# Optimization experiments

Hardware: AMD Instinct MI355X
Metric: run time of the kernel (lower is better)

The kernel has to match this reference:

```python
import jax, jax.numpy as jnp
import numpy as np

AGENT_RADIUS = 0.3
B, F, H1, H21, H22, C, K = 262144, 5, 128, 32, 32, 2, 8


def _linear_init(k, fan_in, fan_out):
    lim = 1.0 / np.sqrt(fan_in)
    kw, kb = jax.random.split(k)
    W = jax.random.uniform(kw, (fan_out, fan_in), jnp.float32, -lim, lim)
    b = jax.random.uniform(kb, (fan_out,), jnp.float32, -lim, lim)
    return W, b


def setup_inputs() -> dict:
    key = jax.random.key(0)
    ks = jax.random.split(key, 9)
    W1, b1 = _linear_init(ks[0], F, H1)
    W21, b21 = _linear_init(ks[1], H1, H21)
    W22, b22 = _linear_init(ks[2], H1, H22)
    W31, b31 = _linear_init(ks[3], H21, C)
    W32, b32 = _linear_init(ks[4], H22, C)
    x = jax.random.normal(ks[5], (B, F), jnp.float32)
    mean = jax.random.normal(ks[6], (F,), jnp.float32) * 0.1
    std = jax.random.uniform(ks[7], (F,), jnp.float32, 0.5, 1.5)
    obs_xy = jax.random.uniform(ks[8], (K, 2), jnp.float32, -10.0, 10.0)
    obstacles = jnp.concatenate([obs_xy, jnp.full((K, 1), 0.5, jnp.float32)], axis=1)  # [K,3] = (ox,oy,r)
    return {"x": x, "mean": mean, "std": std,
            "W1": W1, "b1": b1, "W21": W21, "b21": b21, "W22": W22, "b22": b22,
            "W31": W31, "b31": b31, "W32": W32, "b32": b32,
            "obstacles": obstacles, "sgn": 1}


def _barriernet(x, mean, std, W1, b1, W21, b21, W22, b22, W31, b31, W32, b32, obstacles):
    nB = x.shape[0]
    x0 = x * std + mean
    h1 = jax.nn.relu(x @ W1.T + b1)                 # [B, H1]
    x21 = jax.nn.relu(h1 @ W21.T + b21)             # [B, H21]
    x22 = jax.nn.relu(h1 @ W22.T + b22)             # [B, H22]
    x31 = x21 @ W31.T + b31                          # [B, 2]  QP linear term p
    x32 = 4.0 * jax.nn.sigmoid(x22 @ W32.T + b32)    # [B, 2]  CBF class-K gains

    xo = x0 * std + mean  # module denormalizes twice inside dCBF (faithful to source)
    px, py, theta = xo[:, 0], xo[:, 1], xo[:, 2]
    oppx, oppy = xo[:, 3], xo[:, 4]
    cos_t, sin_t = jnp.cos(theta), jnp.sin(theta)

    # K static obstacles (broadcast) + 1 per-sample opponent -> nobs = K+1
    ox = jnp.concatenate([jnp.broadcast_to(obstacles[:, 0], (nB, K)), oppx[:, None]], axis=1)
    oy = jnp.concatenate([jnp.broadcast_to(obstacles[:, 1], (nB, K)), oppy[:, None]], axis=1)
    orr = jnp.concatenate([jnp.broadcast_to(obstacles[:, 2], (nB, K)),
                           jnp.full((nB, 1), AGENT_RADIUS, x.dtype)], axis=1)
    dx = px[:, None] - ox                            # [B, nobs]
    dy = py[:, None] - oy
    barrier = dx * dx + dy * dy - orr * orr          # [B, nobs]
    LgLf1 = 2.0 * dx * cos_t[:, None] + 2.0 * dy * sin_t[:, None]

    # QP: min 0.5 u^T I u + p^T u  s.t.  g1*u1 <= h  (second G column is 0)
    g1 = -LgLf1                                      # [B, nobs]
    hvec = (x32[:, 0] * x32[:, 1])[:, None] * barrier
    safe_g = jnp.where(g1 != 0.0, g1, 1.0)
    ratio = hvec / safe_g
    upper = jnp.min(jnp.where(g1 > 0.0, ratio, jnp.inf), axis=1)   # tightest u1 upper bound
    lower = jnp.max(jnp.where(g1 < 0.0, ratio, -jnp.inf), axis=1)  # tightest u1 lower bound
    u1 = jnp.clip(-x31[:, 0], lower, upper)          # exact KKT solution of the 1-D QP
    u2 = -x31[:, 1]                                  # unconstrained coordinate
    return jnp.stack([u1, u2], axis=1)               # [B, 2]


def reference(x, mean, std, W1, b1, W21, b21, W22, b22, W31, b31, W32, b32, obstacles, sgn):
    return _barriernet(x, mean, std, W1, b1, W21, b21, W22, b22, W31, b31, W32, b32, obstacles)
```

## Files before the change

### kernel.cpp

```cpp
#include <hip/hip_runtime.h>
#include <math.h>

typedef __attribute__((ext_vector_type(8))) short short8v;
typedef __attribute__((ext_vector_type(4))) float f32x4;

#define BLOCK 256
#define GRID  512

__device__ inline unsigned int pk_bf16(float lo, float hi) {
    unsigned int r;
    asm("v_cvt_pk_bf16_f32 %0, %1, %2" : "=v"(r) : "v"(lo), "v"(hi));
    return r;
}
__device__ inline short8v as_s8(uint4 v) { union { uint4 u; short8v s; } c; c.u = v; return c.s; }
__device__ inline f32x4 as_f4(float4 v) { union { float4 u; f32x4 s; } c; c.u = v; return c.s; }

__global__ __launch_bounds__(BLOCK, 2) void bnet(
    const float* __restrict__ x,
    const float* __restrict__ meanp, const float* __restrict__ stdp,
    const float* __restrict__ W1,  const float* __restrict__ b1,
    const float* __restrict__ W21, const float* __restrict__ b21,
    const float* __restrict__ W22, const float* __restrict__ b22,
    const float* __restrict__ W31, const float* __restrict__ b31,
    const float* __restrict__ W32, const float* __restrict__ b32,
    const float* __restrict__ obstacles,
    float* __restrict__ out, int nB)
{
    __shared__ uint4 w1frag[8 * 64];
    __shared__ uint4 fragB[16 * 64];
    __shared__ uint4 headA[2 * 64];
    __shared__ float b2s[64];

    const int t = threadIdx.x;

    {
        uint4 z = {0u, 0u, 0u, 0u};
        w1frag[t] = z; w1frag[t + 256] = z;
    }
    __syncthreads();
    if (t < 128) {
        int m = t & 15, g = t >> 4;
        int u = 16 * g + m;
        const float* wr = W1 + u * 5;
        uint4 v;
        v.x = pk_bf16(wr[0], wr[1]);
        v.y = pk_bf16(wr[2], wr[3]);
        v.z = pk_bf16(wr[4], b1[u]);
        v.w = 0u;
        w1frag[g * 64 + m] = v;
    } else {
        int e  = t - 128;
        int ks = e >> 6, l = e & 63, m = l & 15, qq = l >> 4;
        float v[8];
        #pragma unroll
        for (int j = 0; j < 8; ++j) {
            int u = 16 * ((j >> 2) & 1) + 4 * qq + (j & 3);
            float val = 0.f;
            if (m == 0 && ks == 0) val = W31[u];
            if (m == 1 && ks == 0) val = W31[32 + u];
            if (m == 2 && ks == 1) val = W32[u];
            if (m == 3 && ks == 1) val = W32[32 + u];
            v[j] = val;
        }
        uint4 h;
        h.x = pk_bf16(v[0], v[1]); h.y = pk_bf16(v[2], v[3]);
        h.z = pk_bf16(v[4], v[5]); h.w = pk_bf16(v[6], v[7]);
        headA[ks * 64 + l] = h;
    }
    if (t < 64) b2s[t] = (t < 32) ? b21[t] : b22[t - 32];
    {
        const float4* w21v = (const float4*)W21;
        const float4* w22v = (const float4*)W22;
        #pragma unroll
        for (int e = 0; e < 4; ++e) {
            int g4   = t + e * 256;
            int uo   = g4 >> 5;
            int h0   = (g4 & 31) << 2;
            int ks   = h0 >> 5;
            int jh   = (h0 >> 4) & 1;
            int qq   = (h0 >> 2) & 3;
            int ln   = (qq << 4) | (uo & 15);
            int half = uo >> 4;
            float4 f1 = w21v[g4];
            float4 f2 = w22v[g4];
            unsigned int* dA = (unsigned int*)&fragB[(half * 4 + ks) * 64 + ln];
            unsigned int* dB = (unsigned int*)&fragB[(8 + half * 4 + ks) * 64 + ln];
            dA[jh * 2] = pk_bf16(f1.x, f1.y); dA[jh * 2 + 1] = pk_bf16(f1.z, f1.w);
            dB[jh * 2] = pk_bf16(f2.x, f2.y); dB[jh * 2 + 1] = pk_bf16(f2.z, f2.w);
        }
    }
    __syncthreads();

    const int lane = t & 63;
    const int q    = lane >> 4;
    const int r15  = lane & 15;
    const int wid    = blockIdx.x * 4 + (t >> 6);
    const int nwaves = GRID * 4;
    const int npairs = (nB + 31) >> 5;
    if (wid >= npairs) return;

    short8v bfr[16];
    #pragma unroll
    for (int i = 0; i < 16; ++i) bfr[i] = as_s8(fragB[i * 64 + lane]);
    const short8v hA0 = as_s8(headA[lane]);
    const short8v hA1 = as_s8(headA[64 + lane]);
    const float4* b2v = (const float4*)b2s;

    const float hb0 = b31[0], hb1 = b31[1], hb2 = b32[0], hb3 = b32[1];

    auto MLP = [&](const float xA[5], const float xB[5], f32x4& hdA, f32x4& hdB) {
        uint4 va, vb;
        va.x = pk_bf16(xA[0], xA[1]); va.y = pk_bf16(xA[2], xA[3]);
        va.z = pk_bf16(xA[4], 1.0f);  va.w = 0u;
        vb.x = pk_bf16(xB[0], xB[1]); vb.y = pk_bf16(xB[2], xB[3]);
        vb.z = pk_bf16(xB[4], 1.0f);  vb.w = 0u;
        short8v xfA = as_s8(va), xfB = as_s8(vb);

        short8v afA[4], afB[4];
        #pragma unroll
        for (int ks = 0; ks < 4; ++ks) {
            f32x4 z = {0.f, 0.f, 0.f, 0.f};
            short8v w0  = as_s8(w1frag[(2 * ks) * 64 + lane]);
            short8v w1v = as_s8(w1frag[(2 * ks + 1) * 64 + lane]);
            f32x4 hA0_ = __builtin_amdgcn_mfma_f32_16x16x32_bf16(w0,  xfA, z, 0, 0, 0);
            f32x4 hA1_ = __builtin_amdgcn_mfma_f32_16x16x32_bf16(w1v, xfA, z, 0, 0, 0);
            f32x4 hB0_ = __builtin_amdgcn_mfma_f32_16x16x32_bf16(w0,  xfB, z, 0, 0, 0);
            f32x4 hB1_ = __builtin_amdgcn_mfma_f32_16x16x32_bf16(w1v, xfB, z, 0, 0, 0);
            uint4 pa, pb;
            pa.x = pk_bf16(fmaxf(hA0_[0], 0.f), fmaxf(hA0_[1], 0.f));
            pa.y = pk_bf16(fmaxf(hA0_[2], 0.f), fmaxf(hA0_[3], 0.f));
            pa.z = pk_bf16(fmaxf(hA1_[0], 0.f), fmaxf(hA1_[1], 0.f));
            pa.w = pk_bf16(fmaxf(hA1_[2], 0.f), fmaxf(hA1_[3], 0.f));
            pb.x = pk_bf16(fmaxf(hB0_[0], 0.f), fmaxf(hB0_[1], 0.f));
            pb.y = pk_bf16(fmaxf(hB0_[2], 0.f), fmaxf(hB0_[3], 0.f));
            pb.z = pk_bf16(fmaxf(hB1_[0], 0.f), fmaxf(hB1_[1], 0.f));
            pb.w = pk_bf16(fmaxf(hB1_[2], 0.f), fmaxf(hB1_[3], 0.f));
            afA[ks] = as_s8(pa); afB[ks] = as_s8(pb);
        }

        f32x4 a21aA = as_f4(b2v[q]);
        f32x4 a21bA = as_f4(b2v[4 + q]);
        f32x4 a22aA = as_f4(b2v[8 + q]);
        f32x4 a22bA = as_f4(b2v[12 + q]);
        f32x4 a21aB = a21aA, a21bB = a21bA, a22aB = a22aA, a22bB = a22bA;
        #pragma unroll
        for (int ks = 0; ks < 4; ++ks) {
            a21aA = __builtin_amdgcn_mfma_f32_16x16x32_bf16(bfr[     ks], afA[ks], a21aA, 0, 0, 0);
            a21aB = __builtin_amdgcn_mfma_f32_16x16x32_bf16(bfr[     ks], afB[ks], a21aB, 0, 0, 0);
            a21bA = __builtin_amdgcn_mfma_f32_16x16x32_bf16(bfr[ 4 + ks], afA[ks], a21bA, 0, 0, 0);
            a21bB = __builtin_amdgcn_mfma_f32_16x16x32_bf16(bfr[ 4 + ks], afB[ks], a21bB, 0, 0, 0);
            a22aA = __builtin_amdgcn_mfma_f32_16x16x32_bf16(bfr[ 8 + ks], afA[ks], a22aA, 0, 0, 0);
            a22aB = __builtin_amdgcn_mfma_f32_16x16x32_bf16(bfr[ 8 + ks], afB[ks], a22aB, 0, 0, 0);
            a22bA = __builtin_amdgcn_mfma_f32_16x16x32_bf16(bfr[12 + ks], afA[ks], a22bA, 0, 0, 0);
            a22bB = __builtin_amdgcn_mfma_f32_16x16x32_bf16(bfr[12 + ks], afB[ks], a22bB, 0, 0, 0);
        }

        uint4 h1A, h2A, h1B, h2B;
        h1A.x = pk_bf16(fmaxf(a21aA[0], 0.f), fmaxf(a21aA[1], 0.f));
        h1A.y = pk_bf16(fmaxf(a21aA[2], 0.f), fmaxf(a21aA[3], 0.f));
        h1A.z = pk_bf16(fmaxf(a21bA[0], 0.f), fmaxf(a21bA[1], 0.f));
        h1A.w = pk_bf16(fmaxf(a21bA[2], 0.f), fmaxf(a21bA[3], 0.f));
        h2A.x = pk_bf16(fmaxf(a22aA[0], 0.f), fmaxf(a22aA[1], 0.f));
        h2A.y = pk_bf16(fmaxf(a22aA[2], 0.f), fmaxf(a22aA[3], 0.f));
        h2A.z = pk_bf16(fmaxf(a22bA[0], 0.f), fmaxf(a22bA[1], 0.f));
        h2A.w = pk_bf16(fmaxf(a22bA[2], 0.f), fmaxf(a22bA[3], 0.f));
        h1B.x = pk_bf16(fmaxf(a21aB[0], 0.f), fmaxf(a21aB[1], 0.f));
        h1B.y = pk_bf16(fmaxf(a21aB[2], 0.f), fmaxf(a21aB[3], 0.f));
        h1B.z = pk_bf16(fmaxf(a21bB[0], 0.f), fmaxf(a21bB[1], 0.f));
        h1B.w = pk_bf16(fmaxf(a21bB[2], 0.f), fmaxf(a21bB[3], 0.f));
        h2B.x = pk_bf16(fmaxf(a22aB[0], 0.f), fmaxf(a22aB[1], 0.f));
        h2B.y = pk_bf16(fmaxf(a22aB[2], 0.f), fmaxf(a22aB[3], 0.f));
        h2B.z = pk_bf16(fmaxf(a22bB[0], 0.f), fmaxf(a22bB[1], 0.f));
        h2B.w = pk_bf16(fmaxf(a22bB[2], 0.f), fmaxf(a22bB[3], 0.f));

        f32x4 ini = {hb0, hb1, hb2, hb3};
        hdA = __builtin_amdgcn_mfma_f32_16x16x32_bf16(hA0, as_s8(h1A), ini, 0, 0, 0);
        hdA = __builtin_amdgcn_mfma_f32_16x16x32_bf16(hA1, as_s8(h2A), hdA, 0, 0, 0);
        hdB = __builtin_amdgcn_mfma_f32_16x16x32_bf16(hA0, as_s8(h1B), ini, 0, 0, 0);
        hdB = __builtin_amdgcn_mfma_f32_16x16x32_bf16(hA1, as_s8(h2B), hdB, 0, 0, 0);
    };

    auto LOADX = [&](int p, float xA[5], float xB[5]) {
        int rA = p * 32 + r15;      if (rA >= nB) rA = nB - 1;
        int rB = p * 32 + 16 + r15; if (rB >= nB) rB = nB - 1;
        const float* pA = x + (size_t)rA * 5;
        const float* pB = x + (size_t)rB * 5;
        #pragma unroll
        for (int c = 0; c < 5; ++c) { xA[c] = pA[c]; xB[c] = pB[c]; }
    };

    int p = wid;
    float xrA[5], xrB[5];
    LOADX(p, xrA, xrB);
    f32x4 hdA, hdB;
    MLP(xrA, xrB, hdA, hdB);

    while (true) {
        const int nxt = p + nwaves;
        const bool has = nxt < npairs;
        float xnA[5], xnB[5];
        if (has) LOADX(nxt, xnA, xnB);

        {
            float hs0 = __shfl(hdB[0], r15);
            float hs1 = __shfl(hdB[1], r15);
            float hs2 = __shfl(hdB[2], r15);
            float hs3 = __shfl(hdB[3], r15);
            if (lane < 32) {
                const bool sa = (lane < 16);
                float x31_0 = sa ? hdA[0] : hs0;
                float x31_1 = sa ? hdA[1] : hs1;
                float t32_0 = sa ? hdA[2] : hs2;
                float t32_1 = sa ? hdA[3] : hs3;

                float s0v = __fdividef(4.f, 1.f + __expf(-t32_0));
                float s1v = __fdividef(4.f, 1.f + __expf(-t32_1));
                float hcoef = s0v * s1v;

                float xo[5];
                #pragma unroll
                for (int c = 0; c < 5; ++c) {
                    float m = meanp[c], s = stdp[c];
                    float xc = sa ? xrA[c] : xrB[c];
                    float x0 = fmaf(xc, s, m);
                    xo[c] = fmaf(x0, s, m);
                }
                float px = xo[0], py = xo[1], th = xo[2], oppx = xo[3], oppy = xo[4];
                float st, ct;
                __sincosf(th, &st, &ct);

                float upper = INFINITY, lower = -INFINITY;
                #pragma unroll
                for (int j = 0; j < 9; ++j) {
                    float ox, oy, rr2;
                    if (j < 8) {
                        ox = obstacles[j * 3];
                        oy = obstacles[j * 3 + 1];
                        float rr = obstacles[j * 3 + 2];
                        rr2 = rr * rr;
                    } else {
                        ox = oppx; oy = oppy; rr2 = 0.3f * 0.3f;
                    }
                    float dx = px - ox, dy = py - oy;
                    float bar = fmaf(dx, dx, fmaf(dy, dy, -rr2));
                    float g1  = -2.f * fmaf(dx, ct, dy * st);
                    float ratio = __fdividef(hcoef * bar, (g1 != 0.f) ? g1 : 1.f);
                    if (g1 > 0.f) upper = fminf(upper, ratio);
                    if (g1 < 0.f) lower = fmaxf(lower, ratio);
                }
                float u1 = fminf(fmaxf(-x31_0, lower), upper);
                float u2 = -x31_1;

                int row = p * 32 + lane;
                if (row < nB) {
                    float2 o; o.x = u1; o.y = u2;
                    *reinterpret_cast<float2*>(out + 2 * (size_t)row) = o;
                }
            }
        }

        if (!has) break;
        MLP(xnA, xnB, hdA, hdB);
        p = nxt;
        #pragma unroll
        for (int c = 0; c < 5; ++c) { xrA[c] = xnA[c]; xrB[c] = xnB[c]; }
    }
}

extern "C" void kernel_launch(void* const* d_in, const int* in_sizes, int n_in,
                              void* d_out, int out_size, void* d_ws, size_t ws_size,
                              hipStream_t stream) {
    const float* x         = (const float*)d_in[0];
    const float* meanp     = (const float*)d_in[1];
    const float* stdp      = (const float*)d_in[2];
    const float* W1        = (const float*)d_in[3];
    const float* b1        = (const float*)d_in[4];
    const float* W21       = (const float*)d_in[5];
    const float* b21       = (const float*)d_in[6];
    const float* W22       = (const float*)d_in[7];
    const float* b22       = (const float*)d_in[8];
    const float* W31       = (const float*)d_in[9];
    const float* b31       = (const float*)d_in[10];
    const float* W32       = (const float*)d_in[11];
    const float* b32       = (const float*)d_in[12];
    const float* obstacles = (const float*)d_in[13];
    float* out = (float*)d_out;

    int nB = in_sizes[0] / 5;
    bnet<<<GRID, BLOCK, 0, stream>>>(
        x, meanp, stdp, W1, b1, W21, b21, W22, b22,
        W31, b31, W32, b32, obstacles, out, nB);
}
```

Baseline: 19.79 us.

## Unroll persistent loop into four fixed pairs with two-pair batched MLP

Replaces the persistent while-loop with a straight-line schedule in which each wave handles exactly four 32-row pairs. The MLP now runs two pairs at once, interleaving the first and second layers per k-step, and epilogues are interleaved with the next MLP batch. The aim is more independent MFMA chains in flight (more ILP) and less loop and prefetch overhead. It raises accumulator register pressure, and it silently assumes the batch needs at most four pairs per wave, so larger inputs would leave rows uncomputed.

```diff
diff --git a/kernel.cpp b/kernel.cpp
--- a/kernel.cpp
+++ b/kernel.cpp
@@ -102,83 +102,11 @@
     short8v bfr[16];
     #pragma unroll
     for (int i = 0; i < 16; ++i) bfr[i] = as_s8(fragB[i * 64 + lane]);
-    const short8v hA0 = as_s8(headA[lane]);
-    const short8v hA1 = as_s8(headA[64 + lane]);
+    const short8v hfr0 = as_s8(headA[lane]);
+    const short8v hfr1 = as_s8(headA[64 + lane]);
     const float4* b2v = (const float4*)b2s;
 
     const float hb0 = b31[0], hb1 = b31[1], hb2 = b32[0], hb3 = b32[1];
-
-    auto MLP = [&](const float xA[5], const float xB[5], f32x4& hdA, f32x4& hdB) {
-        uint4 va, vb;
-        va.x = pk_bf16(xA[0], xA[1]); va.y = pk_bf16(xA[2], xA[3]);
-        va.z = pk_bf16(xA[4], 1.0f);  va.w = 0u;
-        vb.x = pk_bf16(xB[0], xB[1]); vb.y = pk_bf16(xB[2], xB[3]);
-        vb.z = pk_bf16(xB[4], 1.0f);  vb.w = 0u;
-        short8v xfA = as_s8(va), xfB = as_s8(vb);
-
-        short8v afA[4], afB[4];
-        #pragma unroll
-        for (int ks = 0; ks < 4; ++ks) {
-            f32x4 z = {0.f, 0.f, 0.f, 0.f};
-            short8v w0  = as_s8(w1frag[(2 * ks) * 64 + lane]);
-            short8v w1v = as_s8(w1frag[(2 * ks + 1) * 64 + lane]);
-            f32x4 hA0_ = __builtin_amdgcn_mfma_f32_16x16x32_bf16(w0,  xfA, z, 0, 0, 0);
-            f32x4 hA1_ = __builtin_amdgcn_mfma_f32_16x16x32_bf16(w1v, xfA, z, 0, 0, 0);
-            f32x4 hB0_ = __builtin_amdgcn_mfma_f32_16x16x32_bf16(w0,  xfB, z, 0, 0, 0);
-            f32x4 hB1_ = __builtin_amdgcn_mfma_f32_16x16x32_bf16(w1v, xfB, z, 0, 0, 0);
-            uint4 pa, pb;
-            pa.x = pk_bf16(fmaxf(hA0_[0], 0.f), fmaxf(hA0_[1], 0.f));
-            pa.y = pk_bf16(fmaxf(hA0_[2], 0.f), fmaxf(hA0_[3], 0.f));
-            pa.z = pk_bf16(fmaxf(hA1_[0], 0.f), fmaxf(hA1_[1], 0.f));
-            pa.w = pk_bf16(fmaxf(hA1_[2], 0.f), fmaxf(hA1_[3], 0.f));
-            pb.x = pk_bf16(fmaxf(hB0_[0], 0.f), fmaxf(hB0_[1], 0.f));
-            pb.y = pk_bf16(fmaxf(hB0_[2], 0.f), fmaxf(hB0_[3], 0.f));
-            pb.z = pk_bf16(fmaxf(hB1_[0], 0.f), fmaxf(hB1_[1], 0.f));
-            pb.w = pk_bf16(fmaxf(hB1_[2], 0.f), fmaxf(hB1_[3], 0.f));
-            afA[ks] = as_s8(pa); afB[ks] = as_s8(pb);
-        }
-
-        f32x4 a21aA = as_f4(b2v[q]);
-        f32x4 a21bA = as_f4(b2v[4 + q]);
-        f32x4 a22aA = as_f4(b2v[8 + q]);
-        f32x4 a22bA = as_f4(b2v[12 + q]);
-        f32x4 a21aB = a21aA, a21bB = a21bA, a22aB = a22aA, a22bB = a22bA;
-        #pragma unroll
-        for (int ks = 0; ks < 4; ++ks) {
-            a21aA = __builtin_amdgcn_mfma_f32_16x16x32_bf16(bfr[     ks], afA[ks], a21aA, 0, 0, 0);
-            a21aB = __builtin_amdgcn_mfma_f32_16x16x32_bf16(bfr[     ks], afB[ks], a21aB, 0, 0, 0);
-            a21bA = __builtin_amdgcn_mfma_f32_16x16x32_bf16(bfr[ 4 + ks], afA[ks], a21bA, 0, 0, 0);
-            a21bB = __builtin_amdgcn_mfma_f32_16x16x32_bf16(bfr[ 4 + ks], afB[ks], a21bB, 0, 0, 0);
-            a22aA = __builtin_amdgcn_mfma_f32_16x16x32_bf16(bfr[ 8 + ks], afA[ks], a22aA, 0, 0, 0);
-            a22aB = __builtin_amdgcn_mfma_f32_16x16x32_bf16(bfr[ 8 + ks], afB[ks], a22aB, 0, 0, 0);
-            a22bA = __builtin_amdgcn_mfma_f32_16x16x32_bf16(bfr[12 + ks], afA[ks], a22bA, 0, 0, 0);
-            a22bB = __builtin_amdgcn_mfma_f32_16x16x32_bf16(bfr[12 + ks], afB[ks], a22bB, 0, 0, 0);
-        }
-
-        uint4 h1A, h2A, h1B, h2B;
-        h1A.x = pk_bf16(fmaxf(a21aA[0], 0.f), fmaxf(a21aA[1], 0.f));
-        h1A.y = pk_bf16(fmaxf(a21aA[2], 0.f), fmaxf(a21aA[3], 0.f));
-        h1A.z = pk_bf16(fmaxf(a21bA[0], 0.f), fmaxf(a21bA[1], 0.f));
-        h1A.w = pk_bf16(fmaxf(a21bA[2], 0.f), fmaxf(a21bA[3], 0.f));
-        h2A.x = pk_bf16(fmaxf(a22aA[0], 0.f), fmaxf(a22aA[1], 0.f));
-        h2A.y = pk_bf16(fmaxf(a22aA[2], 0.f), fmaxf(a22aA[3], 0.f));
-        h2A.z = pk_bf16(fmaxf(a22bA[0], 0.f), fmaxf(a22bA[1], 0.f));
-        h2A.w = pk_bf16(fmaxf(a22bA[2], 0.f), fmaxf(a22bA[3], 0.f));
-        h1B.x = pk_bf16(fmaxf(a21aB[0], 0.f), fmaxf(a21aB[1], 0.f));
-        h1B.y = pk_bf16(fmaxf(a21aB[2], 0.f), fmaxf(a21aB[3], 0.f));
-        h1B.z = pk_bf16(fmaxf(a21bB[0], 0.f), fmaxf(a21bB[1], 0.f));
-        h1B.w = pk_bf16(fmaxf(a21bB[2], 0.f), fmaxf(a21bB[3], 0.f));
-        h2B.x = pk_bf16(fmaxf(a22aB[0], 0.f), fmaxf(a22aB[1], 0.f));
-        h2B.y = pk_bf16(fmaxf(a22aB[2], 0.f), fmaxf(a22aB[3], 0.f));
-        h2B.z = pk_bf16(fmaxf(a22bB[0], 0.f), fmaxf(a22bB[1], 0.f));
-        h2B.w = pk_bf16(fmaxf(a22bB[2], 0.f), fmaxf(a22bB[3], 0.f));
-
-        f32x4 ini = {hb0, hb1, hb2, hb3};
-        hdA = __builtin_amdgcn_mfma_f32_16x16x32_bf16(hA0, as_s8(h1A), ini, 0, 0, 0);
-        hdA = __builtin_amdgcn_mfma_f32_16x16x32_bf16(hA1, as_s8(h2A), hdA, 0, 0, 0);
-        hdB = __builtin_amdgcn_mfma_f32_16x16x32_bf16(hA0, as_s8(h1B), ini, 0, 0, 0);
-        hdB = __builtin_amdgcn_mfma_f32_16x16x32_bf16(hA1, as_s8(h2B), hdB, 0, 0, 0);
-    };
 
     auto LOADX = [&](int p, float xA[5], float xB[5]) {
         int rA = p * 32 + r15;      if (rA >= nB) rA = nB - 1;
@@ -189,82 +117,209 @@
         for (int c = 0; c < 5; ++c) { xA[c] = pA[c]; xB[c] = pB[c]; }
     };
 
-    int p = wid;
-    float xrA[5], xrB[5];
-    LOADX(p, xrA, xrB);
-    f32x4 hdA, hdB;
-    MLP(xrA, xrB, hdA, hdB);
-
-    while (true) {
-        const int nxt = p + nwaves;
-        const bool has = nxt < npairs;
-        float xnA[5], xnB[5];
-        if (has) LOADX(nxt, xnA, xnB);
-
+    auto MLP4 = [&](const float xA0[5], const float xB0[5],
+                    const float xA1[5], const float xB1[5],
+                    f32x4& hd0A, f32x4& hd0B, f32x4& hd1A, f32x4& hd1B) {
+        uint4 t0a, t0b, t1a, t1b;
+        t0a.x = pk_bf16(xA0[0], xA0[1]); t0a.y = pk_bf16(xA0[2], xA0[3]);
+        t0a.z = pk_bf16(xA0[4], 1.0f);   t0a.w = 0u;
+        t0b.x = pk_bf16(xB0[0], xB0[1]); t0b.y = pk_bf16(xB0[2], xB0[3]);
+        t0b.z = pk_bf16(xB0[4], 1.0f);   t0b.w = 0u;
+        t1a.x = pk_bf16(xA1[0], xA1[1]); t1a.y = pk_bf16(xA1[2], xA1[3]);
+        t1a.z = pk_bf16(xA1[4], 1.0f);   t1a.w = 0u;
+        t1b.x = pk_bf16(xB1[0], xB1[1]); t1b.y = pk_bf16(xB1[2], xB1[3]);
+        t1b.z = pk_bf16(xB1[4], 1.0f);   t1b.w = 0u;
+        short8v xf0A = as_s8(t0a), xf0B = as_s8(t0b);
+        short8v xf1A = as_s8(t1a), xf1B = as_s8(t1b);
+
+        f32x4 i0 = as_f4(b2v[q]),     i1 = as_f4(b2v[4 + q]);
+        f32x4 i2 = as_f4(b2v[8 + q]), i3 = as_f4(b2v[12 + q]);
+        f32x4 A0_21a = i0, A0_21b = i1, A0_22a = i2, A0_22b = i3;
+        f32x4 B0_21a = i0, B0_21b = i1, B0_22a = i2, B0_22b = i3;
+        f32x4 A1_21a = i0, A1_21b = i1, A1_22a = i2, A1_22b = i3;
+        f32x4 B1_21a = i0, B1_21b = i1, B1_22a = i2, B1_22b = i3;
+
+        #pragma unroll
+        for (int ks = 0; ks < 4; ++ks) {
+            f32x4 z = {0.f, 0.f, 0.f, 0.f};
+            short8v w0  = as_s8(w1frag[(2 * ks) * 64 + lane]);
+            short8v w1v = as_s8(w1frag[(2 * ks + 1) * 64 + lane]);
+            f32x4 u0A = __builtin_amdgcn_mfma_f32_16x16x32_bf16(w0,  xf0A, z, 0, 0, 0);
+            f32x4 v0A = __builtin_amdgcn_mfma_f32_16x16x32_bf16(w1v, xf0A, z, 0, 0, 0);
+            f32x4 u0B = __builtin_amdgcn_mfma_f32_16x16x32_bf16(w0,  xf0B, z, 0, 0, 0);
+            f32x4 v0B = __builtin_amdgcn_mfma_f32_16x16x32_bf16(w1v, xf0B, z, 0, 0, 0);
+            f32x4 u1A = __builtin_amdgcn_mfma_f32_16x16x32_bf16(w0,  xf1A, z, 0, 0, 0);
+            f32x4 v1A = __builtin_amdgcn_mfma_f32_16x16x32_bf16(w1v, xf1A, z, 0, 0, 0);
+            f32x4 u1B = __builtin_amdgcn_mfma_f32_16x16x32_bf16(w0,  xf1B, z, 0, 0, 0);
+            f32x4 v1B = __builtin_amdgcn_mfma_f32_16x16x32_bf16(w1v, xf1B, z, 0, 0, 0);
+            uint4 pa, pb, pc, pd;
+            pa.x = pk_bf16(fmaxf(u0A[0], 0.f), fmaxf(u0A[1], 0.f));
+            pa.y = pk_bf16(fmaxf(u0A[2], 0.f), fmaxf(u0A[3], 0.f));
+            pa.z = pk_bf16(fmaxf(v0A[0], 0.f), fmaxf(v0A[1], 0.f));
+            pa.w = pk_bf16(fmaxf(v0A[2], 0.f), fmaxf(v0A[3], 0.f));
+            pb.x = pk_bf16(fmaxf(u0B[0], 0.f), fmaxf(u0B[1], 0.f));
+            pb.y = pk_bf16(fmaxf(u0B[2], 0.f), fmaxf(u0B[3], 0.f));
+            pb.z = pk_bf16(fmaxf(v0B[0], 0.f), fmaxf(v0B[1], 0.f));
+            pb.w = pk_bf16(fmaxf(v0B[2], 0.f), fmaxf(v0B[3], 0.f));
+            pc.x = pk_bf16(fmaxf(u1A[0], 0.f), fmaxf(u1A[1], 0.f));
+            pc.y = pk_bf16(fmaxf(u1A[2], 0.f), fmaxf(u1A[3], 0.f));
+            pc.z = pk_bf16(fmaxf(v1A[0], 0.f), fmaxf(v1A[1], 0.f));
+            pc.w = pk_bf16(fmaxf(v1A[2], 0.f), fmaxf(v1A[3], 0.f));
+            pd.x = pk_bf16(fmaxf(u1B[0], 0.f), fmaxf(u1B[1], 0.f));
+            pd.y = pk_bf16(fmaxf(u1B[2], 0.f), fmaxf(u1B[3], 0.f));
+            pd.z = pk_bf16(fmaxf(v1B[0], 0.f), fmaxf(v1B[1], 0.f));
+            pd.w = pk_bf16(fmaxf(v1B[2], 0.f), fmaxf(v1B[3], 0.f));
+            short8v af0A = as_s8(pa), af0B = as_s8(pb);
+            short8v af1A = as_s8(pc), af1B = as_s8(pd);
+            A0_21a = __builtin_amdgcn_mfma_f32_16x16x32_bf16(bfr[     ks], af0A, A0_21a, 0, 0, 0);
+            B0_21a = __builtin_amdgcn_mfma_f32_16x16x32_bf16(bfr[     ks], af0B, B0_21a, 0, 0, 0);
+            A1_21a = __builtin_amdgcn_mfma_f32_16x16x32_bf16(bfr[     ks], af1A, A1_21a, 0, 0, 0);
+            B1_21a = __builtin_amdgcn_mfma_f32_16x16x32_bf16(bfr[     ks], af1B, B1_21a, 0, 0, 0);
+            A0_21b = __builtin_amdgcn_mfma_f32_16x16x32_bf16(bfr[ 4 + ks], af0A, A0_21b, 0, 0, 0);
+            B0_21b = __builtin_amdgcn_mfma_f32_16x16x32_bf16(bfr[ 4 + ks], af0B, B0_21b, 0, 0, 0);
+            A1_21b = __builtin_amdgcn_mfma_f32_16x16x32_bf16(bfr[ 4 + ks], af1A, A1_21b, 0, 0, 0);
+            B1_21b = __builtin_amdgcn_mfma_f32_16x16x32_bf16(bfr[ 4 + ks], af1B, B1_21b, 0, 0, 0);
+            A0_22a = __builtin_amdgcn_mfma_f32_16x16x32_bf16(bfr[ 8 + ks], af0A, A0_22a, 0, 0, 0);
+            B0_22a = __builtin_amdgcn_mfma_f32_16x16x32_bf16(bfr[ 8 + ks], af0B, B0_22a, 0, 0, 0);
+            A1_22a = __builtin_amdgcn_mfma_f32_16x16x32_bf16(bfr[ 8 + ks], af1A, A1_22a, 0, 0, 0);
+            B1_22a = __builtin_amdgcn_mfma_f32_16x16x32_bf16(bfr[ 8 + ks], af1B, B1_22a, 0, 0, 0);
+            A0_22b = __builtin_amdgcn_mfma_f32_16x16x32_bf16(bfr[12 + ks], af0A, A0_22b, 0, 0, 0);
+            B0_22b = __builtin_amdgcn_mfma_f32_16x16x32_bf16(bfr[12 + ks], af0B, B0_22b, 0, 0, 0);
+            A1_22b = __builtin_amdgcn_mfma_f32_16x16x32_bf16(bfr[12 + ks], af1A, A1_22b, 0, 0, 0);
+            B1_22b = __builtin_amdgcn_mfma_f32_16x16x32_bf16(bfr[12 + ks], af1B, B1_22b, 0, 0, 0);
+        }
+
+        f32x4 ini = {hb0, hb1, hb2, hb3};
         {
-            float hs0 = __shfl(hdB[0], r15);
-            float hs1 = __shfl(hdB[1], r15);
-            float hs2 = __shfl(hdB[2], r15);
-            float hs3 = __shfl(hdB[3], r15);
-            if (lane < 32) {
-                const bool sa = (lane < 16);
-                float x31_0 = sa ? hdA[0] : hs0;
-                float x31_1 = sa ? hdA[1] : hs1;
-                float t32_0 = sa ? hdA[2] : hs2;
-                float t32_1 = sa ? hdA[3] : hs3;
-
-                float s0v = __fdividef(4.f, 1.f + __expf(-t32_0));
-                float s1v = __fdividef(4.f, 1.f + __expf(-t32_1));
-                float hcoef = s0v * s1v;
-
-                float xo[5];
-                #pragma unroll
-                for (int c = 0; c < 5; ++c) {
-                    float m = meanp[c], s = stdp[c];
-                    float xc = sa ? xrA[c] : xrB[c];
-                    float x0 = fmaf(xc, s, m);
-                    xo[c] = fmaf(x0, s, m);
+            uint4 h1, h2;
+            h1.x = pk_bf16(fmaxf(A0_21a[0], 0.f), fmaxf(A0_21a[1], 0.f));
+            h1.y = pk_bf16(fmaxf(A0_21a[2], 0.f), fmaxf(A0_21a[3], 0.f));
+            h1.z = pk_bf16(fmaxf(A0_21b[0], 0.f), fmaxf(A0_21b[1], 0.f));
+            h1.w = pk_bf16(fmaxf(A0_21b[2], 0.f), fmaxf(A0_21b[3], 0.f));
+            h2.x = pk_bf16(fmaxf(A0_22a[0], 0.f), fmaxf(A0_22a[1], 0.f));
+            h2.y = pk_bf16(fmaxf(A0_22a[2], 0.f), fmaxf(A0_22a[3], 0.f));
+            h2.z = pk_bf16(fmaxf(A0_22b[0], 0.f), fmaxf(A0_22b[1], 0.f));
+            h2.w = pk_bf16(fmaxf(A0_22b[2], 0.f), fmaxf(A0_22b[3], 0.f));
+            hd0A = __builtin_amdgcn_mfma_f32_16x16x32_bf16(hfr0, as_s8(h1), ini, 0, 0, 0);
+            hd0A = __builtin_amdgcn_mfma_f32_16x16x32_bf16(hfr1, as_s8(h2), hd0A, 0, 0, 0);
+        }
+        {
+            uint4 h1, h2;
+            h1.x = pk_bf16(fmaxf(B0_21a[0], 0.f), fmaxf(B0_21a[1], 0.f));
+            h1.y = pk_bf16(fmaxf(B0_21a[2], 0.f), fmaxf(B0_21a[3], 0.f));
+            h1.z = pk_bf16(fmaxf(B0_21b[0], 0.f), fmaxf(B0_21b[1], 0.f));
+            h1.w = pk_bf16(fmaxf(B0_21b[2], 0.f), fmaxf(B0_21b[3], 0.f));
+            h2.x = pk_bf16(fmaxf(B0_22a[0], 0.f), fmaxf(B0_22a[1], 0.f));
+            h2.y = pk_bf16(fmaxf(B0_22a[2], 0.f), fmaxf(B0_22a[3], 0.f));
+            h2.z = pk_bf16(fmaxf(B0_22b[0], 0.f), fmaxf(B0_22b[1], 0.f));
+            h2.w = pk_bf16(fmaxf(B0_22b[2], 0.f), fmaxf(B0_22b[3], 0.f));
+            hd0B = __builtin_amdgcn_mfma_f32_16x16x32_bf16(hfr0, as_s8(h1), ini, 0, 0, 0);
+            hd0B = __builtin_amdgcn_mfma_f32_16x16x32_bf16(hfr1, as_s8(h2), hd0B, 0, 0, 0);
+        }
+        {
+            uint4 h1, h2;
+            h1.x = pk_bf16(fmaxf(A1_21a[0], 0.f), fmaxf(A1_21a[1], 0.f));
+            h1.y = pk_bf16(fmaxf(A1_21a[2], 0.f), fmaxf(A1_21a[3], 0.f));
+            h1.z = pk_bf16(fmaxf(A1_21b[0], 0.f), fmaxf(A1_21b[1], 0.f));
+            h1.w = pk_bf16(fmaxf(A1_21b[2], 0.f), fmaxf(A1_21b[3], 0.f));
+            h2.x = pk_bf16(fmaxf(A1_22a[0], 0.f), fmaxf(A1_22a[1], 0.f));
+            h2.y = pk_bf16(fmaxf(A1_22a[2], 0.f), fmaxf(A1_22a[3], 0.f));
+            h2.z = pk_bf16(fmaxf(A1_22b[0], 0.f), fmaxf(A1_22b[1], 0.f));
+            h2.w = pk_bf16(fmaxf(A1_22b[2], 0.f), fmaxf(A1_22b[3], 0.f));
+            hd1A = __builtin_amdgcn_mfma_f32_16x16x32_bf16(hfr0, as_s8(h1), ini, 0, 0, 0);
+            hd1A = __builtin_amdgcn_mfma_f32_16x16x32_bf16(hfr1, as_s8(h2), hd1A, 0, 0, 0);
+        }
+        {
+            uint4 h1, h2;
+            h1.x = pk_bf16(fmaxf(B1_21a[0], 0.f), fmaxf(B1_21a[1], 0.f));
+            h1.y = pk_bf16(fmaxf(B1_21a[2], 0.f), fmaxf(B1_21a[3], 0.f));
+            h1.z = pk_bf16(fmaxf(B1_21b[0], 0.f), fmaxf(B1_21b[1], 0.f));
+            h1.w = pk_bf16(fmaxf(B1_21b[2], 0.f), fmaxf(B1_21b[3], 0.f));
+            h2.x = pk_bf16(fmaxf(B1_22a[0], 0.f), fmaxf(B1_22a[1], 0.f));
+            h2.y = pk_bf16(fmaxf(B1_22a[2], 0.f), fmaxf(B1_22a[3], 0.f));
+            h2.z = pk_bf16(fmaxf(B1_22b[0], 0.f), fmaxf(B1_22b[1], 0.f));
+            h2.w = pk_bf16(fmaxf(B1_22b[2], 0.f), fmaxf(B1_22b[3], 0.f));
+            hd1B = __builtin_amdgcn_mfma_f32_16x16x32_bf16(hfr0, as_s8(h1), ini, 0, 0, 0);
+            hd1B = __builtin_amdgcn_mfma_f32_16x16x32_bf16(hfr1, as_s8(h2), hd1B, 0, 0, 0);
+        }
+    };
+
+    auto EPI = [&](int p, const float xA[5], const float xB[5],
+                   const f32x4& hdA, const f32x4& hdB) {
+        float hs0 = __shfl(hdB[0], r15);
+        float hs1 = __shfl(hdB[1], r15);
+        float hs2 = __shfl(hdB[2], r15);
+        float hs3 = __shfl(hdB[3], r15);
+        if (lane < 32) {
+            const bool sa = (lane < 16);
+            float x31_0 = sa ? hdA[0] : hs0;
+            float x31_1 = sa ? hdA[1] : hs1;
+            float t32_0 = sa ? hdA[2] : hs2;
+            float t32_1 = sa ? hdA[3] : hs3;
+
+            float s0v = __fdividef(4.f, 1.f + __expf(-t32_0));
+            float s1v = __fdividef(4.f, 1.f + __expf(-t32_1));
+            float hcoef = s0v * s1v;
+
+            float xo[5];
+            #pragma unroll
+            for (int c = 0; c < 5; ++c) {
+                float m = meanp[c], s = stdp[c];
+                float xc = sa ? xA[c] : xB[c];
+                float x0 = fmaf(xc, s, m);
+                xo[c] = fmaf(x0, s, m);
+            }
+            float px = xo[0], py = xo[1], th = xo[2], oppx = xo[3], oppy = xo[4];
+            float st, ct;
+            __sincosf(th, &st, &ct);
+
+            float upper = INFINITY, lower = -INFINITY;
+            #pragma unroll
+            for (int j = 0; j < 9; ++j) {
+                float ox, oy, rr2;
+                if (j < 8) {
+                    ox = obstacles[j * 3];
+                    oy = obstacles[j * 3 + 1];
+                    float rr = obstacles[j * 3 + 2];
+                    rr2 = rr * rr;
+                } else {
+                    ox = oppx; oy = oppy; rr2 = 0.3f * 0.3f;
                 }
-                float px = xo[0], py = xo[1], th = xo[2], oppx = xo[3], oppy = xo[4];
-                float st, ct;
-                __sincosf(th, &st, &ct);
-
-                float upper = INFINITY, lower = -INFINITY;
-                #pragma unroll
-                for (int j = 0; j < 9; ++j) {
-                    float ox, oy, rr2;
-                    if (j < 8) {
-                        ox = obstacles[j * 3];
-                        oy = obstacles[j * 3 + 1];
-                        float rr = obstacles[j * 3 + 2];
-                        rr2 = rr * rr;
-                    } else {
-                        ox = oppx; oy = oppy; rr2 = 0.3f * 0.3f;
-                    }
-                    float dx = px - ox, dy = py - oy;
-                    float bar = fmaf(dx, dx, fmaf(dy, dy, -rr2));
-                    float g1  = -2.f * fmaf(dx, ct, dy * st);
-                    float ratio = __fdividef(hcoef * bar, (g1 != 0.f) ? g1 : 1.f);
-                    if (g1 > 0.f) upper = fminf(upper, ratio);
-                    if (g1 < 0.f) lower = fmaxf(lower, ratio);
-                }
-                float u1 = fminf(fmaxf(-x31_0, lower), upper);
-                float u2 = -x31_1;
-
-                int row = p * 32 + lane;
-                if (row < nB) {
-                    float2 o; o.x = u1; o.y = u2;
-                    *reinterpret_cast<float2*>(out + 2 * (size_t)row) = o;
-                }
+                float dx = px - ox, dy = py - oy;
+                float bar = fmaf(dx, dx, fmaf(dy, dy, -rr2));
+                float g1  = -2.f * fmaf(dx, ct, dy * st);
+                float ratio = __fdividef(hcoef * bar, (g1 != 0.f) ? g1 : 1.f);
+                if (g1 > 0.f) upper = fminf(upper, ratio);
+                if (g1 < 0.f) lower = fmaxf(lower, ratio);
             }
-        }
-
-        if (!has) break;
-        MLP(xnA, xnB, hdA, hdB);
-        p = nxt;
-        #pragma unroll
-        for (int c = 0; c < 5; ++c) { xrA[c] = xnA[c]; xrB[c] = xnB[c]; }
-    }
+            float u1 = fminf(fmaxf(-x31_0, lower), upper);
+            float u2 = -x31_1;
+
+            int row = p * 32 + lane;
+            if (row < nB) {
+                float2 o; o.x = u1; o.y = u2;
+                *reinterpret_cast<float2*>(out + 2 * (size_t)row) = o;
+            }
+        }
+    };
+
+    const int P0 = wid;
+    const int P1 = wid + nwaves;
+    const int P2 = wid + 2 * nwaves;
+    const int P3 = wid + 3 * nwaves;
+
+    float x0A[5], x0B[5], x1A[5], x1B[5], x2A[5], x2B[5], x3A[5], x3B[5];
+    LOADX(P0, x0A, x0B);
+    LOADX(P1, x1A, x1B);
+    f32x4 hd0A, hd0B, hd1A, hd1B, hd2A, hd2B, hd3A, hd3B;
+    MLP4(x0A, x0B, x1A, x1B, hd0A, hd0B, hd1A, hd1B);
+    LOADX(P2, x2A, x2B);
+    LOADX(P3, x3A, x3B);
+    EPI(P0, x0A, x0B, hd0A, hd0B);
+    MLP4(x2A, x2B, x3A, x3B, hd2A, hd2B, hd3A, hd3B);
+    EPI(P1, x1A, x1B, hd1A, hd1B);
+    EPI(P2, x2A, x2B, hd2A, hd2B);
+    EPI(P3, x3A, x3B, hd3A, hd3B);
 }
 
 extern "C" void kernel_launch(void* const* d_in, const int* in_sizes, int n_in,
```

After: 19.47 us. Within noise of the previous version (-1.6%).
